# Kernel tuning notes

Measured on AMD Instinct MI355X. Metric: run time of the kernel, lower is better.

Reference implementation:

```python
import jax, jax.numpy as jnp
import numpy as np
import math

B, T, H, D = 4, 2048, 16, 64
C = H * D            # d_model = 1024
FF = 4096            # mlp_hidden_dim
N_LAYERS = 12
EPS = 1e-5


def setup_inputs() -> dict:
    key = jax.random.key(0)
    ks = jax.random.split(key, 8)
    res_scale = 1.0 / math.sqrt(2 * N_LAYERS)
    std_c = math.sqrt(2.0 / C)
    std_ff = math.sqrt(2.0 / FF)
    return {
        "x": jax.random.normal(ks[0], (B, T, C), jnp.float32),
        "ln1_w": jnp.ones((C,), jnp.float32),
        "ln1_b": jnp.zeros((C,), jnp.float32),
        # weights stored [in, out] (transposed vs torch nn.Linear.weight)
        "w_qkv": jax.random.normal(ks[1], (C, 3 * C), jnp.float32) * std_c,
        "b_qkv": jnp.zeros((3 * C,), jnp.float32),
        "w_o": jax.random.normal(ks[2], (C, C), jnp.float32) * std_c * res_scale,
        "b_o": jnp.zeros((C,), jnp.float32),
        "ln2_w": jnp.ones((C,), jnp.float32),
        "ln2_b": jnp.zeros((C,), jnp.float32),
        "w_fc": jax.random.normal(ks[3], (C, FF), jnp.float32) * std_c,
        "b_fc": jnp.zeros((FF,), jnp.float32),
        "w_out": jax.random.normal(ks[4], (FF, C), jnp.float32) * std_ff * res_scale,
        "b_out": jnp.zeros((C,), jnp.float32),
    }


def _layer_norm(x, w, b):
    m = jnp.mean(x, axis=-1, keepdims=True)
    v = jnp.mean(jnp.square(x - m), axis=-1, keepdims=True)
    return (x - m) * jax.lax.rsqrt(v + EPS) * w + b


def reference(x, ln1_w, ln1_b, w_qkv, b_qkv, w_o, b_o, ln2_w, ln2_b, w_fc, b_fc, w_out, b_out):
    Bx, Tx, Cx = x.shape
    # attention
    qkv = _layer_norm(x, ln1_w, ln1_b) @ w_qkv + b_qkv          # [B,T,3C]
    q, k, v = jnp.split(qkv, 3, axis=-1)
    q = q.reshape(Bx, Tx, H, D)
    k = k.reshape(Bx, Tx, H, D)
    v = v.reshape(Bx, Tx, H, D)
    att = jnp.einsum("bqhd,bkhd->bhqk", q, k) / math.sqrt(D)    # [B,H,T,T]
    mask = jnp.tril(jnp.ones((Tx, Tx), dtype=bool))
    att = jnp.where(mask, att, -jnp.inf)
    att = jax.nn.softmax(att, axis=-1)
    y = jnp.einsum("bhqk,bkhd->bqhd", att, v).reshape(Bx, Tx, Cx)
    x = x + y @ w_o + b_o
    # mlp (torch F.gelu default = exact erf gelu)
    h = jax.nn.gelu(_layer_norm(x, ln2_w, ln2_b) @ w_fc + b_fc, approximate=False)
    x = x + h @ w_out + b_out
    return x
```

## Files before the change

### kernel.cpp

```cpp
#include <hip/hip_runtime.h>
#include <hip/hip_bf16.h>
#include <cstdint>


#define B_ 4
#define T_ 2048
#define H_ 16
#define D_ 64
#define C_ 1024
#define FF_ 4096
#define M_ (B_ * T_)
#define QKV_N (3 * C_)

typedef __bf16 bf16x8 __attribute__((ext_vector_type(8)));
typedef __bf16 bf16x4 __attribute__((ext_vector_type(4)));
typedef float floatx4 __attribute__((ext_vector_type(4)));

#define MFMA16(a, b, c) __builtin_amdgcn_mfma_f32_16x16x32_bf16(a, b, c, 0, 0, 0)

__device__ __forceinline__ void gload16(const void* g, void* l) {
  __builtin_amdgcn_global_load_lds(
      (const __attribute__((address_space(1))) void*)g,
      (__attribute__((address_space(3))) void*)l, 16, 0, 0);
}

__device__ __forceinline__ void lds_fence() {
  asm volatile("s_waitcnt lgkmcnt(0)" ::: "memory");
}

__device__ __forceinline__ float gelu_f(float v) {
  return 0.5f * v * (1.0f + erff(v * 0.70710678118654752f));
}

__global__ __launch_bounds__(256) void convert_transpose(
    const float* __restrict__ w, __bf16* __restrict__ wt, int K, int N) {
  __shared__ float tile[32][33];
  const int n0 = blockIdx.x * 32, k0 = blockIdx.y * 32;
  const int tx = threadIdx.x & 31, ty = threadIdx.x >> 5;
#pragma unroll
  for (int i = 0; i < 4; ++i)
    tile[ty + i * 8][tx] = w[(size_t)(k0 + ty + i * 8) * N + n0 + tx];
  __syncthreads();
#pragma unroll
  for (int i = 0; i < 4; ++i)
    wt[(size_t)(n0 + ty + i * 8) * K + k0 + tx] = (__bf16)tile[tx][ty + i * 8];
}

__global__ __launch_bounds__(256) void ln_kernel(
    const float* __restrict__ x, const float* __restrict__ w,
    const float* __restrict__ b, __bf16* __restrict__ out) {
  __shared__ float red[4];
  const int row = blockIdx.x, tid = threadIdx.x;
  const float4 v = ((const float4*)(x + (size_t)row * C_))[tid];
  float s = v.x + v.y + v.z + v.w;
#pragma unroll
  for (int off = 1; off < 64; off <<= 1) s += __shfl_xor(s, off, 64);
  if ((tid & 63) == 0) red[tid >> 6] = s;
  __syncthreads();
  const float mean = (red[0] + red[1] + red[2] + red[3]) * (1.0f / C_);
  __syncthreads();
  const float dx = v.x - mean, dy = v.y - mean, dz = v.z - mean, dw = v.w - mean;
  float s2 = dx * dx + dy * dy + dz * dz + dw * dw;
#pragma unroll
  for (int off = 1; off < 64; off <<= 1) s2 += __shfl_xor(s2, off, 64);
  if ((tid & 63) == 0) red[tid >> 6] = s2;
  __syncthreads();
  const float var = (red[0] + red[1] + red[2] + red[3]) * (1.0f / C_);
  const float rstd = rsqrtf(var + 1e-5f);
  const float4 wv = ((const float4*)w)[tid];
  const float4 bv = ((const float4*)b)[tid];
  bf16x4 o;
  o[0] = (__bf16)(dx * rstd * wv.x + bv.x);
  o[1] = (__bf16)(dy * rstd * wv.y + bv.y);
  o[2] = (__bf16)(dz * rstd * wv.z + bv.z);
  o[3] = (__bf16)(dw * rstd * wv.w + bv.w);
  *(bf16x4*)(out + (size_t)row * C_ + tid * 4) = o;
}

template <bool GELU, bool RESID, bool OUTBF16>
__global__ __launch_bounds__(256, 2) void gemm_kernel(
    const __bf16* __restrict__ A, const __bf16* __restrict__ BT,
    const float* __restrict__ bias, const float* __restrict__ resid,
    float* __restrict__ outF, __bf16* __restrict__ outB, int M, int N, int K) {
  __shared__ __bf16 As[128 * 32];
  __shared__ __bf16 Bs[128 * 32];
  const int tid = threadIdx.x;
  const int wave = tid >> 6, lane = tid & 63;
  const int lane15 = lane & 15, quad = lane >> 4;

  const int gx = gridDim.x, gy = gridDim.y;
  const int linear = blockIdx.y * gx + blockIdx.x;
  const int xcd = linear & 7, idx = linear >> 3;
  const int bn = idx % gx;
  const int bm = xcd * (gy >> 3) + idx / gx;

  const int m0 = bm * 128, n0 = bn * 128;
  const int wm = (wave >> 1) * 64, wn = (wave & 1) * 64;
  const int srow_in_chunk = lane >> 2;
  const int skc = (lane & 3) * 8;

  floatx4 acc[4][4] = {};

  for (int k0 = 0; k0 < K; k0 += 32) {
#pragma unroll
    for (int t = 0; t < 2; ++t) {
      const int chunk = wave * 2 + t;
      const int row = chunk * 16 + srow_in_chunk;
      gload16(A + (size_t)(m0 + row) * K + k0 + skc, &As[chunk * 512]);
      gload16(BT + (size_t)(n0 + row) * K + k0 + skc, &Bs[chunk * 512]);
    }
    __syncthreads();
    bf16x8 af[4], bfr[4];
#pragma unroll
    for (int i = 0; i < 4; ++i) {
      af[i] = *(const bf16x8*)&As[(wm + i * 16 + lane15) * 32 + quad * 8];
      bfr[i] = *(const bf16x8*)&Bs[(wn + i * 16 + lane15) * 32 + quad * 8];
    }
#pragma unroll
    for (int i = 0; i < 4; ++i)
#pragma unroll
      for (int j = 0; j < 4; ++j) acc[i][j] = MFMA16(af[i], bfr[j], acc[i][j]);
    __syncthreads();
  }

#pragma unroll
  for (int mi = 0; mi < 4; ++mi) {
    const int row = m0 + wm + mi * 16 + quad * 4;
#pragma unroll
    for (int ni = 0; ni < 4; ++ni) {
      const int col = n0 + wn + ni * 16 + lane15;
      const float bsum = bias[col];
#pragma unroll
      for (int r = 0; r < 4; ++r) {
        const size_t idx2 = (size_t)(row + r) * N + col;
        float v = acc[mi][ni][r] + bsum;
        if (GELU) v = gelu_f(v);
        if (RESID) v += resid[idx2];
        if (OUTBF16) outB[idx2] = (__bf16)v;
        else outF[idx2] = v;
      }
    }
  }
}

template <bool GELU, bool RESID, bool OUTBF16>
__global__ __launch_bounds__(256, 4) void gemm_n64_kernel(
    const __bf16* __restrict__ A, const __bf16* __restrict__ BT,
    const float* __restrict__ bias, const float* __restrict__ resid,
    float* __restrict__ outF, __bf16* __restrict__ outB, int M, int N, int K) {
  __shared__ __bf16 As[128 * 32];
  __shared__ __bf16 Bs[64 * 32];
  const int tid = threadIdx.x;
  const int wave = tid >> 6, lane = tid & 63;
  const int lane15 = lane & 15, quad = lane >> 4;

  const int gx = gridDim.x, gy = gridDim.y;
  const int linear = blockIdx.y * gx + blockIdx.x;
  const int xcd = linear & 7, idx = linear >> 3;
  const int bn = idx % gx;
  const int bm = xcd * (gy >> 3) + idx / gx;

  const int m0 = bm * 128, n0 = bn * 64;
  const int wm = (wave >> 1) * 64, wn = (wave & 1) * 32;
  const int srow_in_chunk = lane >> 2;
  const int skc = (lane & 3) * 8;

  floatx4 acc[4][2] = {};

  for (int k0 = 0; k0 < K; k0 += 32) {
#pragma unroll
    for (int t = 0; t < 2; ++t) {
      const int chunk = wave * 2 + t;
      const int row = chunk * 16 + srow_in_chunk;
      gload16(A + (size_t)(m0 + row) * K + k0 + skc, &As[chunk * 512]);
    }
    {
      const int row = wave * 16 + srow_in_chunk;
      gload16(BT + (size_t)(n0 + row) * K + k0 + skc, &Bs[wave * 512]);
    }
    __syncthreads();
    bf16x8 af[4], bfr[2];
#pragma unroll
    for (int i = 0; i < 4; ++i)
      af[i] = *(const bf16x8*)&As[(wm + i * 16 + lane15) * 32 + quad * 8];
#pragma unroll
    for (int j = 0; j < 2; ++j)
      bfr[j] = *(const bf16x8*)&Bs[(wn + j * 16 + lane15) * 32 + quad * 8];
#pragma unroll
    for (int i = 0; i < 4; ++i)
#pragma unroll
      for (int j = 0; j < 2; ++j) acc[i][j] = MFMA16(af[i], bfr[j], acc[i][j]);
    __syncthreads();
  }

#pragma unroll
  for (int mi = 0; mi < 4; ++mi) {
    const int row = m0 + wm + mi * 16 + quad * 4;
#pragma unroll
    for (int ni = 0; ni < 2; ++ni) {
      const int col = n0 + wn + ni * 16 + lane15;
      const float bsum = bias[col];
#pragma unroll
      for (int r = 0; r < 4; ++r) {
        const size_t idx2 = (size_t)(row + r) * N + col;
        float v = acc[mi][ni][r] + bsum;
        if (GELU) v = gelu_f(v);
        if (RESID) v += resid[idx2];
        if (OUTBF16) outB[idx2] = (__bf16)v;
        else outF[idx2] = v;
      }
    }
  }
}

#define PT_S 72
#define VT_S 72
__global__ __launch_bounds__(256, 4) void attn_kernel(
    const __bf16* __restrict__ qkv, __bf16* __restrict__ y) {
  const int linear = blockIdx.x;
  const int xcd = linear & 7, idx = linear >> 3;
  const int pair = idx & 15;
  const int bh = xcd * 8 + (idx >> 4);
  const int b = bh >> 4, h = bh & 15;

  const int tid = threadIdx.x, wave = tid >> 6, lane = tid & 63;
  const int lane15 = lane & 15, quad = lane >> 4;
  __shared__ __bf16 K0[2][64 * 32];
  __shared__ __bf16 K1[2][64 * 32];
  __shared__ __bf16 Vt[64 * VT_S];
  __shared__ __bf16 Pt[4][16 * PT_S];

  const int krow_loc = lane >> 2;
  const int kdc = (lane & 3) * 8;
  const int v_kv = tid & 63;
  const int v_d0 = (tid >> 6) * 16;
  const float QSCALE = 0.125f * 1.44269504088896f;

  const int qt_of[2] = {pair, 31 - pair};

  bf16x8 onesf;
#pragma unroll
  for (int j = 0; j < 8; ++j) onesf[j] = (__bf16)1.0f;

  bf16x8 vr0, vr1;
  int g = 0;

  {
    const size_t gk =
        (size_t)(b * T_ + wave * 16 + krow_loc) * QKV_N + C_ + h * 64 + kdc;
    gload16(qkv + gk, &K0[0][wave * 16 * 32]);
    gload16(qkv + gk + 32, &K1[0][wave * 16 * 32]);
    const __bf16* vsrc =
        qkv + (size_t)(b * T_ + v_kv) * QKV_N + 2 * C_ + h * 64 + v_d0;
    vr0 = *(const bf16x8*)vsrc;
    vr1 = *(const bf16x8*)(vsrc + 8);
  }

#pragma unroll
  for (int seg = 0; seg < 2; ++seg) {
    const int qt = qt_of[seg];
    const int qrow0 = qt * 64 + wave * 16;

    bf16x8 qf0, qf1;
    {
      const size_t base =
          (size_t)(b * T_ + qrow0 + lane15) * QKV_N + h * 64 + quad * 8;
      const bf16x8 r0 = *(const bf16x8*)(qkv + base);
      const bf16x8 r1 = *(const bf16x8*)(qkv + base + 32);
#pragma unroll
      for (int j = 0; j < 8; ++j) {
        qf0[j] = (__bf16)((float)r0[j] * QSCALE);
        qf1[j] = (__bf16)((float)r1[j] * QSCALE);
      }
    }

    floatx4 o[4] = {};
    floatx4 o4 = {0.f, 0.f, 0.f, 0.f};

    const int ntiles = qt + 1;
    for (int kvt = 0; kvt < ntiles; ++kvt) {
      const int buf = g & 1;
      const int c0 = kvt * 64;
      __syncthreads();
#pragma unroll
      for (int j = 0; j < 8; ++j) {
        Vt[(v_d0 + j) * VT_S + v_kv] = vr0[j];
        Vt[(v_d0 + 8 + j) * VT_S + v_kv] = vr1[j];
      }
      __syncthreads();

      if (!(seg == 1 && kvt + 1 >= ntiles)) {
        const int nkvt = (kvt + 1 >= ntiles) ? 0 : kvt + 1;
        const int nc0 = nkvt * 64;
        const int nbuf = (g + 1) & 1;
        const size_t gk = (size_t)(b * T_ + nc0 + wave * 16 + krow_loc) * QKV_N +
                          C_ + h * 64 + kdc;
        gload16(qkv + gk, &K0[nbuf][wave * 16 * 32]);
        gload16(qkv + gk + 32, &K1[nbuf][wave * 16 * 32]);
        const __bf16* vsrc = qkv + (size_t)(b * T_ + nc0 + v_kv) * QKV_N +
                             2 * C_ + h * 64 + v_d0;
        vr0 = *(const bf16x8*)vsrc;
        vr1 = *(const bf16x8*)(vsrc + 8);
      }

      float p[4][4];
#pragma unroll
      for (int nt = 0; nt < 4; ++nt) {
        const bf16x8 kf0 =
            *(const bf16x8*)&K0[buf][(nt * 16 + lane15) * 32 + quad * 8];
        const bf16x8 kf1 =
            *(const bf16x8*)&K1[buf][(nt * 16 + lane15) * 32 + quad * 8];
        floatx4 s = {0.f, 0.f, 0.f, 0.f};
        s = MFMA16(qf0, kf0, s);
        s = MFMA16(qf1, kf1, s);
#pragma unroll
        for (int r = 0; r < 4; ++r) p[nt][r] = s[r];
      }
      if (kvt == qt) {
#pragma unroll
        for (int nt = 0; nt < 4; ++nt) {
          const int tk = c0 + nt * 16 + lane15;
#pragma unroll
          for (int r = 0; r < 4; ++r) {
            const int tq = qrow0 + quad * 4 + r;
            p[nt][r] = (tk <= tq) ? p[nt][r] : -1e30f;
          }
        }
      }

#pragma unroll
      for (int nt = 0; nt < 4; ++nt)
#pragma unroll
        for (int r = 0; r < 4; ++r)
          Pt[wave][(quad * 4 + r) * PT_S + nt * 16 + lane15] =
              (__bf16)__builtin_amdgcn_exp2f(p[nt][r]);
      lds_fence();

#pragma unroll
      for (int half = 0; half < 2; ++half) {
        const bf16x8 pf =
            *(const bf16x8*)&Pt[wave][lane15 * PT_S + half * 32 + quad * 8];
#pragma unroll
        for (int dt = 0; dt < 4; ++dt) {
          const bf16x8 vf =
              *(const bf16x8*)&Vt[(dt * 16 + lane15) * VT_S + half * 32 + quad * 8];
          o[dt] = MFMA16(pf, vf, o[dt]);
        }
        o4 = MFMA16(pf, onesf, o4);
      }
      ++g;
    }

#pragma unroll
    for (int r = 0; r < 4; ++r) {
      const int tq = qrow0 + quad * 4 + r;
      const float inv = 1.0f / o4[r];
#pragma unroll
      for (int dt = 0; dt < 4; ++dt)
        y[(size_t)(b * T_ + tq) * C_ + h * 64 + dt * 16 + lane15] =
            (__bf16)(o[dt][r] * inv);
    }
  }
}

extern "C" void kernel_launch(void* const* d_in, const int* in_sizes, int n_in,
                              void* d_out, int out_size, void* d_ws,
                              size_t ws_size, hipStream_t stream) {
  const float* x     = (const float*)d_in[0];
  const float* ln1_w = (const float*)d_in[1];
  const float* ln1_b = (const float*)d_in[2];
  const float* w_qkv = (const float*)d_in[3];
  const float* b_qkv = (const float*)d_in[4];
  const float* w_o   = (const float*)d_in[5];
  const float* b_o   = (const float*)d_in[6];
  const float* ln2_w = (const float*)d_in[7];
  const float* ln2_b = (const float*)d_in[8];
  const float* w_fc  = (const float*)d_in[9];
  const float* b_fc  = (const float*)d_in[10];
  const float* w_out = (const float*)d_in[11];
  const float* b_out = (const float*)d_in[12];

  char* ws = (char*)d_ws;
  __bf16* wqkvT = (__bf16*)(ws + 0);
  __bf16* woT   = (__bf16*)(ws + 6291456);
  __bf16* wfcT  = (__bf16*)(ws + 8388608);
  __bf16* woutT = (__bf16*)(ws + 16777216);
  __bf16* xn    = (__bf16*)(ws + 25165824);
  __bf16* qkv   = (__bf16*)(ws + 41943040);
  __bf16* yb    = (__bf16*)(ws + 92274688);
  float*  x1    = (float*)(ws + 109051904);
  __bf16* hb    = (__bf16*)(ws + 142606336);

  convert_transpose<<<dim3(QKV_N / 32, C_ / 32), 256, 0, stream>>>(w_qkv, wqkvT, C_, QKV_N);
  convert_transpose<<<dim3(C_ / 32, C_ / 32), 256, 0, stream>>>(w_o, woT, C_, C_);
  convert_transpose<<<dim3(FF_ / 32, C_ / 32), 256, 0, stream>>>(w_fc, wfcT, C_, FF_);
  convert_transpose<<<dim3(C_ / 32, FF_ / 32), 256, 0, stream>>>(w_out, woutT, FF_, C_);

  ln_kernel<<<M_, 256, 0, stream>>>(x, ln1_w, ln1_b, xn);
  gemm_kernel<false, false, true><<<dim3(QKV_N / 128, M_ / 128), 256, 0, stream>>>(
      xn, wqkvT, b_qkv, nullptr, nullptr, qkv, M_, QKV_N, C_);
  attn_kernel<<<1024, 256, 0, stream>>>(qkv, yb);
  gemm_n64_kernel<false, true, false><<<dim3(C_ / 64, M_ / 128), 256, 0, stream>>>(
      yb, woT, b_o, x, x1, nullptr, M_, C_, C_);
  ln_kernel<<<M_, 256, 0, stream>>>(x1, ln2_w, ln2_b, xn);
  gemm_kernel<true, false, true><<<dim3(FF_ / 128, M_ / 128), 256, 0, stream>>>(
      xn, wfcT, b_fc, nullptr, nullptr, hb, M_, FF_, C_);
  gemm_n64_kernel<false, true, false><<<dim3(C_ / 64, M_ / 128), 256, 0, stream>>>(
      hb, woutT, b_out, x1, (float*)d_out, nullptr, M_, C_, FF_);
}
```

Measured before the change: 524.8 us.

## Double GEMM K-tile to 64 with XOR-swizzled LDS layout

Both GEMM kernels now stage 64-wide K slices per iteration instead of 32. This halves the number of barrier pairs per output tile. The global-to-LDS copies place each 16-byte chunk at an XOR-swizzled column (column ^ row&7), and the fragment reads apply the same swizzle, so LDS reads avoid bank conflicts. LDS usage per block doubles, which may limit occupancy. A leftover unused row computation remains in the n64 kernel.

Measured after the change: 521.5 us. No clear change (-0.6%).

```diff
diff --git a/kernel.cpp b/kernel.cpp
--- a/kernel.cpp
+++ b/kernel.cpp
@@ -77,16 +77,18 @@
   *(bf16x4*)(out + (size_t)row * C_ + tid * 4) = o;
 }
 
+
 template <bool GELU, bool RESID, bool OUTBF16>
 __global__ __launch_bounds__(256, 2) void gemm_kernel(
     const __bf16* __restrict__ A, const __bf16* __restrict__ BT,
     const float* __restrict__ bias, const float* __restrict__ resid,
     float* __restrict__ outF, __bf16* __restrict__ outB, int M, int N, int K) {
-  __shared__ __bf16 As[128 * 32];
-  __shared__ __bf16 Bs[128 * 32];
+  __shared__ __bf16 As[128 * 64];
+  __shared__ __bf16 Bs[128 * 64];
   const int tid = threadIdx.x;
   const int wave = tid >> 6, lane = tid & 63;
   const int lane15 = lane & 15, quad = lane >> 4;
+  const int r7 = lane15 & 7;
 
   const int gx = gridDim.x, gy = gridDim.y;
   const int linear = blockIdx.y * gx + blockIdx.x;
@@ -96,30 +98,35 @@
 
   const int m0 = bm * 128, n0 = bn * 128;
   const int wm = (wave >> 1) * 64, wn = (wave & 1) * 64;
-  const int srow_in_chunk = lane >> 2;
-  const int skc = (lane & 3) * 8;
+
+  const int srow = lane >> 3;
+  const int gc8 = (lane & 7) ^ srow;
 
   floatx4 acc[4][4] = {};
 
-  for (int k0 = 0; k0 < K; k0 += 32) {
-#pragma unroll
-    for (int t = 0; t < 2; ++t) {
-      const int chunk = wave * 2 + t;
-      const int row = chunk * 16 + srow_in_chunk;
-      gload16(A + (size_t)(m0 + row) * K + k0 + skc, &As[chunk * 512]);
-      gload16(BT + (size_t)(n0 + row) * K + k0 + skc, &Bs[chunk * 512]);
+  for (int k0 = 0; k0 < K; k0 += 64) {
+#pragma unroll
+    for (int t = 0; t < 4; ++t) {
+      const int row = wave * 32 + t * 8;
+      gload16(A + (size_t)(m0 + row + srow) * K + k0 + gc8 * 8, &As[row * 64]);
+      gload16(BT + (size_t)(n0 + row + srow) * K + k0 + gc8 * 8, &Bs[row * 64]);
     }
     __syncthreads();
-    bf16x8 af[4], bfr[4];
-#pragma unroll
-    for (int i = 0; i < 4; ++i) {
-      af[i] = *(const bf16x8*)&As[(wm + i * 16 + lane15) * 32 + quad * 8];
-      bfr[i] = *(const bf16x8*)&Bs[(wn + i * 16 + lane15) * 32 + quad * 8];
-    }
-#pragma unroll
-    for (int i = 0; i < 4; ++i)
-#pragma unroll
-      for (int j = 0; j < 4; ++j) acc[i][j] = MFMA16(af[i], bfr[j], acc[i][j]);
+#pragma unroll
+    for (int kk8 = 0; kk8 < 8; kk8 += 4) {
+      bf16x8 af[4], bfr[4];
+#pragma unroll
+      for (int i = 0; i < 4; ++i) {
+        af[i] = *(const bf16x8*)
+            &As[(wm + i * 16 + lane15) * 64 + (((kk8 + quad) ^ r7) << 3)];
+        bfr[i] = *(const bf16x8*)
+            &Bs[(wn + i * 16 + lane15) * 64 + (((kk8 + quad) ^ r7) << 3)];
+      }
+#pragma unroll
+      for (int i = 0; i < 4; ++i)
+#pragma unroll
+        for (int j = 0; j < 4; ++j) acc[i][j] = MFMA16(af[i], bfr[j], acc[i][j]);
+    }
     __syncthreads();
   }
 
@@ -148,11 +155,12 @@
     const __bf16* __restrict__ A, const __bf16* __restrict__ BT,
     const float* __restrict__ bias, const float* __restrict__ resid,
     float* __restrict__ outF, __bf16* __restrict__ outB, int M, int N, int K) {
-  __shared__ __bf16 As[128 * 32];
-  __shared__ __bf16 Bs[64 * 32];
+  __shared__ __bf16 As[128 * 64];
+  __shared__ __bf16 Bs[64 * 64];
   const int tid = threadIdx.x;
   const int wave = tid >> 6, lane = tid & 63;
   const int lane15 = lane & 15, quad = lane >> 4;
+  const int r7 = lane15 & 7;
 
   const int gx = gridDim.x, gy = gridDim.y;
   const int linear = blockIdx.y * gx + blockIdx.x;
@@ -162,34 +170,43 @@
 
   const int m0 = bm * 128, n0 = bn * 64;
   const int wm = (wave >> 1) * 64, wn = (wave & 1) * 32;
-  const int srow_in_chunk = lane >> 2;
-  const int skc = (lane & 3) * 8;
+
+  const int srow = lane >> 3;
+  const int gc8 = (lane & 7) ^ srow;
 
   floatx4 acc[4][2] = {};
 
-  for (int k0 = 0; k0 < K; k0 += 32) {
+  for (int k0 = 0; k0 < K; k0 += 64) {
+#pragma unroll
+    for (int t = 0; t < 4; ++t) {
+      const int row = wave * 32 + t * 8;
+      gload16(A + (size_t)(m0 + row + srow) * K + k0 + gc8 * 8, &As[row * 64]);
+    }
+    {
+      const int row = wave * 16 + (lane >> 3 & 8) + ((lane >> 3) & 7);
+    }
 #pragma unroll
     for (int t = 0; t < 2; ++t) {
-      const int chunk = wave * 2 + t;
-      const int row = chunk * 16 + srow_in_chunk;
-      gload16(A + (size_t)(m0 + row) * K + k0 + skc, &As[chunk * 512]);
-    }
-    {
-      const int row = wave * 16 + srow_in_chunk;
-      gload16(BT + (size_t)(n0 + row) * K + k0 + skc, &Bs[wave * 512]);
+      const int row = wave * 16 + t * 8;
+      gload16(BT + (size_t)(n0 + row + srow) * K + k0 + gc8 * 8, &Bs[row * 64]);
     }
     __syncthreads();
-    bf16x8 af[4], bfr[2];
-#pragma unroll
-    for (int i = 0; i < 4; ++i)
-      af[i] = *(const bf16x8*)&As[(wm + i * 16 + lane15) * 32 + quad * 8];
-#pragma unroll
-    for (int j = 0; j < 2; ++j)
-      bfr[j] = *(const bf16x8*)&Bs[(wn + j * 16 + lane15) * 32 + quad * 8];
-#pragma unroll
-    for (int i = 0; i < 4; ++i)
-#pragma unroll
-      for (int j = 0; j < 2; ++j) acc[i][j] = MFMA16(af[i], bfr[j], acc[i][j]);
+#pragma unroll
+    for (int kk8 = 0; kk8 < 8; kk8 += 4) {
+      bf16x8 af[4], bfr[2];
+#pragma unroll
+      for (int i = 0; i < 4; ++i)
+        af[i] = *(const bf16x8*)
+            &As[(wm + i * 16 + lane15) * 64 + (((kk8 + quad) ^ r7) << 3)];
+#pragma unroll
+      for (int j = 0; j < 2; ++j)
+        bfr[j] = *(const bf16x8*)
+            &Bs[(wn + j * 16 + lane15) * 64 + (((kk8 + quad) ^ r7) << 3)];
+#pragma unroll
+      for (int i = 0; i < 4; ++i)
+#pragma unroll
+        for (int j = 0; j < 2; ++j) acc[i][j] = MFMA16(af[i], bfr[j], acc[i][j]);
+    }
     __syncthreads();
   }
 
```
